# Optimization experiments

Hardware: AMD Instinct MI355X
Metric: run time of the kernel (lower is better)

## Reference

```python
import jax, jax.numpy as jnp
import numpy as np

NUM_EXPERTS = 16
TOP_K = 8
INIT_STD = 0.02

def setup_inputs() -> dict:
    key = jax.random.key(0)
    ks = jax.random.split(key, 5)
    B, S, H, I, E = 2, 2048, 2048, 768, NUM_EXPERTS
    return {
        "hidden_states": jax.random.normal(ks[0], (B, S, H), jnp.float32),
        "w_router": jax.random.normal(ks[1], (H, E), jnp.float32) * INIT_STD,
        "w_gate": jax.random.normal(ks[2], (E, H, I), jnp.float32) * INIT_STD,
        "w_up": jax.random.normal(ks[3], (E, H, I), jnp.float32) * INIT_STD,
        "w_down": jax.random.normal(ks[4], (E, I, H), jnp.float32) * INIT_STD,
    }

def reference(hidden_states, w_router, w_gate, w_up, w_down):
    # Router: logits -> fp32 softmax -> top-k -> renormalize (norm_topk_prob=True)
    router_logits = jnp.einsum("bsh,he->bse", hidden_states, w_router)  # [B,S,E]
    routing_weights = jax.nn.softmax(router_logits.astype(jnp.float32), axis=-1)
    topk_w, topk_idx = jax.lax.top_k(routing_weights, k=TOP_K)  # [B,S,K]
    topk_w = topk_w / topk_w.sum(axis=-1, keepdims=True)
    # Dense per-expert combine weights [B,S,E] (sum over top-k slots matching each expert)
    dense_w = jnp.sum(jax.nn.one_hot(topk_idx, NUM_EXPERTS, dtype=topk_w.dtype) * topk_w[..., None], axis=2)
    dense_w = dense_w.astype(hidden_states.dtype)
    # Every expert runs on all tokens (as in the source loop), vectorized over E
    gate = jax.nn.silu(jnp.einsum("bsh,ehi->besi", hidden_states, w_gate))  # [B,E,S,I]
    up = jnp.einsum("bsh,ehi->besi", hidden_states, w_up)
    expert_out = jnp.einsum("besi,eih->besh", gate * up, w_down)  # [B,E,S,H]
    final = jnp.einsum("bse,besh->bsh", dense_w, expert_out)
    return final, router_logits
```

## Files before the change

kernel.cpp:

```cpp
#include <hip/hip_runtime.h>
#include <hip/hip_bf16.h>


typedef __attribute__((ext_vector_type(8))) short short8;
typedef __attribute__((ext_vector_type(4))) float f32x4;
typedef __attribute__((ext_vector_type(4))) unsigned short us4;

#define NUM_T 4096
#define DH    2048
#define DI    768
#define NE    16
#define DKD   (NE*DI)
#define MAXMT 20
#define HSC_CAP 2560
#define TOK_HALF 2048
#define FINAL_ELEMS ((size_t)NUM_T*DH)


static __device__ __forceinline__ unsigned short f2bf(float f) {
  unsigned int u = __builtin_bit_cast(unsigned int, f);
  u += 0x7fffu + ((u >> 16) & 1u);
  return (unsigned short)(u >> 16);
}

static __device__ __forceinline__ float bf2f(unsigned short b) {
  unsigned int u = ((unsigned int)b) << 16;
  return __builtin_bit_cast(float, u);
}

static __device__ __forceinline__ void gload16(const void* g, void* l) {
  __builtin_amdgcn_global_load_lds(
      (__attribute__((address_space(1))) void*)(g),
      (__attribute__((address_space(3))) void*)(l), 16, 0, 0);
}


__global__ __launch_bounds__(256)
void cvt_hidden_k(const float* __restrict__ in, unsigned short* __restrict__ out) {
  size_t i = (size_t)blockIdx.x * 256 + threadIdx.x;
  const float4* p = (const float4*)in + i * 2;
  float4 a = p[0], b = p[1];
  short8 v;
  v[0] = (short)f2bf(a.x); v[1] = (short)f2bf(a.y);
  v[2] = (short)f2bf(a.z); v[3] = (short)f2bf(a.w);
  v[4] = (short)f2bf(b.x); v[5] = (short)f2bf(b.y);
  v[6] = (short)f2bf(b.z); v[7] = (short)f2bf(b.w);
  *(short8*)(out + i * 8) = v;
}


__global__ __launch_bounds__(256)
void transpose_cvt_k(const float* __restrict__ s0, unsigned short* __restrict__ d0,
                     const float* __restrict__ s1, unsigned short* __restrict__ d1,
                     int C, long inStrideE, long outStrideE, int outLD) {
  __shared__ float tile[128][33];
  const int zz = blockIdx.z, e = zz & 15;
  const float* inE = (zz < 16 ? s0 : s1) + (size_t)e * inStrideE;
  unsigned short* outE = (zz < 16 ? d0 : d1) + (size_t)e * outStrideE;
  const int r0 = blockIdx.x * 128, c0 = blockIdx.y * 32;
  const int tid = threadIdx.x;
  const int lc = tid & 31, rg = tid >> 5;
#pragma unroll
  for (int i = 0; i < 16; i++)
    tile[rg * 16 + i][lc] = inE[(size_t)(r0 + rg * 16 + i) * C + c0 + lc];
  __syncthreads();
  const int u = tid & 31, cg = tid >> 5;
#pragma unroll
  for (int i = 0; i < 4; i++) {
    int c = cg * 4 + i;
    us4 v;
    v[0] = f2bf(tile[u * 4 + 0][c]); v[1] = f2bf(tile[u * 4 + 1][c]);
    v[2] = f2bf(tile[u * 4 + 2][c]); v[3] = f2bf(tile[u * 4 + 3][c]);
    *(us4*)(outE + (size_t)(c0 + c) * outLD + r0 + u * 4) = v;
  }
}


__global__ __launch_bounds__(256)
void router_k(const float* __restrict__ x, const float* __restrict__ wr,
              float* __restrict__ logits_out, unsigned short* __restrict__ dwb,
              unsigned char* __restrict__ slt) {
  int t = blockIdx.x;
  int tid = threadIdx.x, lane = tid & 63, wid = tid >> 6;
  float acc[16];
#pragma unroll
  for (int e = 0; e < 16; e++) acc[e] = 0.f;
  const float* xt = x + (size_t)t * DH;
  for (int i = tid; i < DH; i += 256) {
    float hv = xt[i];
    const float4* w4 = (const float4*)(wr + (size_t)i * 16);
#pragma unroll
    for (int q = 0; q < 4; q++) {
      float4 w = w4[q];
      acc[q * 4 + 0] += hv * w.x; acc[q * 4 + 1] += hv * w.y;
      acc[q * 4 + 2] += hv * w.z; acc[q * 4 + 3] += hv * w.w;
    }
  }
#pragma unroll
  for (int e = 0; e < 16; e++) {
#pragma unroll
    for (int off = 32; off; off >>= 1) acc[e] += __shfl_xor(acc[e], off, 64);
  }
  __shared__ float red[4][16];
  if (lane == 0) {
#pragma unroll
    for (int e = 0; e < 16; e++) red[wid][e] = acc[e];
  }
  __syncthreads();
  if (tid == 0) {
    float lg[16];
#pragma unroll
    for (int e = 0; e < 16; e++) lg[e] = red[0][e] + red[1][e] + red[2][e] + red[3][e];
    float mx = lg[0];
#pragma unroll
    for (int e = 1; e < 16; e++) mx = fmaxf(mx, lg[e]);
    float p[16], s = 0.f;
#pragma unroll
    for (int e = 0; e < 16; e++) { p[e] = __expf(lg[e] - mx); s += p[e]; }
    float inv = 1.f / s;
#pragma unroll
    for (int e = 0; e < 16; e++) p[e] *= inv;
    float tmp[16];
#pragma unroll
    for (int e = 0; e < 16; e++) tmp[e] = p[e];
    int idx[8]; float val[8]; float ts = 0.f;
#pragma unroll
    for (int k = 0; k < 8; k++) {
      int b = 0; float bv = tmp[0];
#pragma unroll
      for (int e = 1; e < 16; e++) { if (tmp[e] > bv) { bv = tmp[e]; b = e; } }
      idx[k] = b; val[k] = bv; tmp[b] = -1.f; ts += bv;
    }
    float dw[16];
    unsigned char sl[16];
#pragma unroll
    for (int e = 0; e < 16; e++) { dw[e] = 0.f; sl[e] = 0xFF; }
    float invt = 1.f / ts;
#pragma unroll
    for (int k = 0; k < 8; k++) { dw[idx[k]] += val[k] * invt; sl[idx[k]] = (unsigned char)k; }
#pragma unroll
    for (int e = 0; e < 16; e++) {
      dwb[(size_t)t * 16 + e] = f2bf(dw[e]);
      slt[(size_t)t * 16 + e] = sl[e];
      logits_out[(size_t)t * 16 + e] = lg[e];
    }
  }
}


__global__ __launch_bounds__(256)
void build_lists_k(const unsigned short* __restrict__ dwb,
                   const unsigned char* __restrict__ slt,
                   unsigned short* __restrict__ lst, int* __restrict__ meta) {
  int e = blockIdx.x;
  int tid = threadIdx.x;
  unsigned short loc[16]; int c = 0;
#pragma unroll
  for (int j = 0; j < 16; j++) {
    int t = tid * 16 + j;
    if (dwb[(size_t)t * 16 + e] != 0) {
      unsigned short s = slt[(size_t)t * 16 + e];
      loc[c++] = (unsigned short)(t | (s << 12));
    }
  }
  __shared__ int sc[256];
  __shared__ int pre[257];
  sc[tid] = c;
  __syncthreads();
  if (tid == 0) {
    int s = 0;
    for (int i = 0; i < 256; i++) { pre[i] = s; s += sc[i]; }
    pre[256] = s;
  }
  __syncthreads();
  unsigned short* L = lst + (size_t)e * NUM_T;
  int base = pre[tid];
  for (int j = 0; j < c; j++) L[base + j] = loc[j];
  int total = pre[256];
  for (int i = total + tid; i < NUM_T; i += 256) L[i] = 0xFFFFu;
  if (tid == 0) { meta[e * 2] = pre[128]; meta[e * 2 + 1] = total; }
}


__global__ __launch_bounds__(256, 3)
void gateup_k(const unsigned short* __restrict__ hbf,
              const unsigned short* __restrict__ wgbt,
              const unsigned short* __restrict__ wubt,
              const unsigned short* __restrict__ dwb,
              const unsigned short* __restrict__ lst,
              unsigned short* __restrict__ hsC) {
  const int bxr = blockIdx.x;
  const int wl  = (bxr & 7) * 480 + (bxr >> 3);
  const int e   = wl / 240;
  const int rem = wl - e * 240;
  const int n0  = (rem / MAXMT) * 64;
  const int m0  = (rem % MAXMT) * 128;

  const unsigned short* L = lst + (size_t)e * NUM_T;
  if (L[m0] & 0x8000) return;

  const int tid = threadIdx.x, lane = tid & 63, wid = tid >> 6;
  const int wm = wid >> 1, wn = wid & 1;
  const int lr = lane & 15, lgp = lane >> 4;

  __shared__ alignas(16) unsigned short As [3 * 128 * 32];
  __shared__ alignas(16) unsigned short Bgs[3 *  64 * 32];
  __shared__ alignas(16) unsigned short Bus[3 *  64 * 32];

  f32x4 zero = {0.f, 0.f, 0.f, 0.f};
  f32x4 accg[4][2], accu[4][2];
#pragma unroll
  for (int m = 0; m < 4; m++)
#pragma unroll
    for (int n = 0; n < 2; n++) { accg[m][n] = zero; accu[m][n] = zero; }

  const unsigned short* wgE = wgbt + (size_t)e * DI * DH;
  const unsigned short* wuE = wubt + (size_t)e * DI * DH;

  const int srow    = lane >> 2;
  const int schunk8 = (((lane & 3) - ((lane >> 3) & 3)) & 3) * 8;

  const int ar0 = m0 + wid * 32 + srow, ar1 = ar0 + 16;
  const unsigned short t0 = L[ar0], t1 = L[ar1];
  const size_t prow0 = (t0 & 0x8000) ? 0 : (size_t)(t0 & 0xFFF);
  const size_t prow1 = (t1 & 0x8000) ? 0 : (size_t)(t1 & 0xFFF);
  const size_t brow = (size_t)(n0 + wid * 16 + srow);

  const int slot8 = (((lane >> 4) + ((lane >> 1) & 3)) & 3) * 8;

  auto stage = [&](int b, int k0) {
    unsigned short* Ab = As  + b * 4096 + wid * 1024;
    unsigned short* Gb = Bgs + b * 2048 + wid * 512;
    unsigned short* Ub = Bus + b * 2048 + wid * 512;
    gload16(hbf + prow0 * DH + k0 + schunk8, Ab);
    gload16(hbf + prow1 * DH + k0 + schunk8, Ab + 512);
    gload16(wgE + brow  * DH + k0 + schunk8, Gb);
    gload16(wuE + brow  * DH + k0 + schunk8, Ub);
  };

  auto compute = [&](int b) {
    const unsigned short* Ab = As  + b * 4096;
    const unsigned short* Gb = Bgs + b * 2048;
    const unsigned short* Ub = Bus + b * 2048;
    short8 a[4], bg[2], bu[2];
#pragma unroll
    for (int m = 0; m < 4; m++)
      a[m] = *(const short8*)(Ab + (wm * 64 + m * 16 + lr) * 32 + slot8);
#pragma unroll
    for (int n = 0; n < 2; n++) {
      bg[n] = *(const short8*)(Gb + (wn * 32 + n * 16 + lr) * 32 + slot8);
      bu[n] = *(const short8*)(Bus + b * 2048 + (wn * 32 + n * 16 + lr) * 32 + slot8);
    }
    (void)Ub;
#pragma unroll
    for (int m = 0; m < 4; m++)
#pragma unroll
      for (int n = 0; n < 2; n++) {
        accg[m][n] = __builtin_amdgcn_mfma_f32_16x16x32_bf16(a[m], bg[n], accg[m][n], 0, 0, 0);
        accu[m][n] = __builtin_amdgcn_mfma_f32_16x16x32_bf16(a[m], bu[n], accu[m][n], 0, 0, 0);
      }
  };

  const int NT = DH / 32;
  stage(0, 0);
  stage(1, 32);
  int bc = 0, bs = 2;
#pragma unroll 1
  for (int i = 0; i < NT - 1; ++i) {
    asm volatile("s_waitcnt vmcnt(4)" ::: "memory");
    __builtin_amdgcn_s_barrier();
    __builtin_amdgcn_sched_barrier(0);
    if (i + 2 < NT) stage(bs, (i + 2) * 32);
    compute(bc);
    bc = (bc == 2) ? 0 : bc + 1;
    bs = (bs == 2) ? 0 : bs + 1;
  }
  asm volatile("s_waitcnt vmcnt(0)" ::: "memory");
  __builtin_amdgcn_s_barrier();
  __builtin_amdgcn_sched_barrier(0);
  compute(bc);

#pragma unroll
  for (int m = 0; m < 4; m++) {
#pragma unroll
    for (int r = 0; r < 4; r++) {
      int mrow = m0 + wm * 64 + m * 16 + 4 * lgp + r;
      unsigned short en = L[mrow];
      if (en & 0x8000) continue;
      int tp = en & 0xFFF;
      float w = bf2f(dwb[(size_t)tp * 16 + e]);
#pragma unroll
      for (int n = 0; n < 2; n++) {
        float g = accg[m][n][r], u = accu[m][n][r];
        float sig = 1.f / (1.f + __expf(-g));
        float val = g * sig * u * w;
        hsC[((size_t)e * HSC_CAP + mrow) * DI + n0 + wn * 32 + n * 16 + lr] = f2bf(val);
      }
    }
  }
}


__global__ __launch_bounds__(256, 3)
void down_half_k(const unsigned short* __restrict__ hsC,
                 const unsigned short* __restrict__ wdbt,
                 const unsigned short* __restrict__ lst,
                 const int* __restrict__ meta,
                 unsigned short* __restrict__ slotbuf, int hf) {
  const int bxr = blockIdx.x;
  const int wl  = (bxr & 7) * 320 + (bxr >> 3);
  const int e   = wl / 160;
  const int rem = wl - e * 160;
  const int n0  = (rem / 10) * 128;
  const int m0  = (rem % 10) * 128;

  const int rs = hf ? meta[e * 2] : 0;
  const int re = hf ? meta[e * 2 + 1] : meta[e * 2];
  const int rcount = re - rs;
  if (m0 >= rcount) return;

  const int tid = threadIdx.x, lane = tid & 63, wid = tid >> 6;
  const int wm = wid >> 1, wn = wid & 1;
  const int lr = lane & 15, lgp = lane >> 4;

  __shared__ alignas(16) unsigned short As[3 * 128 * 32];
  __shared__ alignas(16) unsigned short Bs[3 * 128 * 32];

  f32x4 zero = {0.f, 0.f, 0.f, 0.f};
  f32x4 acc[4][4];
#pragma unroll
  for (int m = 0; m < 4; m++)
#pragma unroll
    for (int n = 0; n < 4; n++) acc[m][n] = zero;

  const int srow    = lane >> 2;
  const int schunk8 = (((lane & 3) - ((lane >> 3) & 3)) & 3) * 8;
  const int sOff0   = wid * 1024;
  const int sOff1   = sOff0 + 512;
  const size_t arow0 = (size_t)(e * HSC_CAP + rs + m0 + wid * 32 + srow);
  const size_t arow1 = arow0 + 16;
  const size_t brow0 = (size_t)(n0 + wid * 32 + srow), brow1 = brow0 + 16;
  const int slot8 = (((lane >> 4) + ((lane >> 1) & 3)) & 3) * 8;

  const unsigned short* wdE = wdbt + (size_t)e * DI;

  auto stage = [&](int b, int k0) {
    unsigned short* Ab = As + b * 4096;
    unsigned short* Bb = Bs + b * 4096;
    gload16(hsC + arow0 * DI + k0 + schunk8, Ab + sOff0);
    gload16(hsC + arow1 * DI + k0 + schunk8, Ab + sOff1);
    gload16(wdE + brow0 * DKD + k0 + schunk8, Bb + sOff0);
    gload16(wdE + brow1 * DKD + k0 + schunk8, Bb + sOff1);
  };

  auto compute = [&](int bsel) {
    const unsigned short* Ab = As + bsel * 4096;
    const unsigned short* Bb = Bs + bsel * 4096;
    short8 a[4], b[4];
#pragma unroll
    for (int m = 0; m < 4; m++)
      a[m] = *(const short8*)(Ab + (size_t)(wm * 64 + m * 16 + lr) * 32 + slot8);
#pragma unroll
    for (int n = 0; n < 4; n++)
      b[n] = *(const short8*)(Bb + (size_t)(wn * 64 + n * 16 + lr) * 32 + slot8);
#pragma unroll
    for (int m = 0; m < 4; m++)
#pragma unroll
      for (int n = 0; n < 4; n++)
        acc[m][n] = __builtin_amdgcn_mfma_f32_16x16x32_bf16(a[m], b[n], acc[m][n], 0, 0, 0);
  };

  const int NT = DI / 32;
  stage(0, 0);
  stage(1, 32);
  int bc = 0, bs = 2;
#pragma unroll 1
  for (int i = 0; i < NT - 1; ++i) {
    asm volatile("s_waitcnt vmcnt(4)" ::: "memory");
    __builtin_amdgcn_s_barrier();
    __builtin_amdgcn_sched_barrier(0);
    if (i + 2 < NT) stage(bs, (i + 2) * 32);
    compute(bc);
    bc = (bc == 2) ? 0 : bc + 1;
    bs = (bs == 2) ? 0 : bs + 1;
  }
  asm volatile("s_waitcnt vmcnt(0)" ::: "memory");
  __builtin_amdgcn_s_barrier();
  __builtin_amdgcn_sched_barrier(0);
  compute(bc);

  const unsigned short* L = lst + (size_t)e * NUM_T;
#pragma unroll
  for (int m = 0; m < 4; m++) {
#pragma unroll
    for (int r = 0; r < 4; r++) {
      int gr = m0 + wm * 64 + m * 16 + 4 * lgp + r;
      if (gr >= rcount) continue;
      unsigned short en = L[rs + gr];
      int t  = en & 0xFFF;
      int s  = (en >> 12) & 7;
      int tl = t - hf * TOK_HALF;
#pragma unroll
      for (int n = 0; n < 4; n++)
        slotbuf[((size_t)s * TOK_HALF + tl) * DH + n0 + wn * 64 + n * 16 + lr] =
            f2bf(acc[m][n][r]);
    }
  }
}


__global__ __launch_bounds__(256)
void reduce_half_k(const unsigned short* __restrict__ slotbuf,
                   float* __restrict__ outp, int hf) {
  size_t i  = (size_t)blockIdx.x * 256 + threadIdx.x;
  size_t tl = i >> 8;
  size_t h0 = (i & 255) * 8;
  float sum[8];
#pragma unroll
  for (int j = 0; j < 8; j++) sum[j] = 0.f;
#pragma unroll
  for (int s = 0; s < 8; s++) {
    short8 v = *(const short8*)(slotbuf + ((size_t)s * TOK_HALF + tl) * DH + h0);
#pragma unroll
    for (int j = 0; j < 8; j++) sum[j] += bf2f((unsigned short)v[j]);
  }
  float* o = outp + ((size_t)(hf * TOK_HALF) + tl) * DH + h0;
  float4 o0 = {sum[0], sum[1], sum[2], sum[3]};
  float4 o1 = {sum[4], sum[5], sum[6], sum[7]};
  *(float4*)o = o0;
  *(float4*)(o + 4) = o1;
}


extern "C" void kernel_launch(void* const* d_in, const int* in_sizes, int n_in,
                              void* d_out, int out_size, void* d_ws, size_t ws_size,
                              hipStream_t stream) {
  const float* x  = (const float*)d_in[0];
  const float* wr = (const float*)d_in[1];
  const float* wg = (const float*)d_in[2];
  const float* wu = (const float*)d_in[3];
  const float* wd = (const float*)d_in[4];

  float* outF = (float*)d_out;
  float* outL = outF + FINAL_ELEMS;

  if (ws_size < 180682880ull) return;
  char* ws = (char*)d_ws;
  unsigned short* hbf   = (unsigned short*)(ws);
  unsigned short* wubt  = (unsigned short*)(ws + 16777216);
  unsigned short* hsC   = (unsigned short*)(ws + 67108864);
  unsigned short* wgbt  = (unsigned short*)(ws + 130023424);
  unsigned short* dwb   = (unsigned short*)(ws + 180355072);
  unsigned short* lst   = (unsigned short*)(ws + 180486144);
  unsigned char*  slt   = (unsigned char*) (ws + 180617216);
  int*            meta  = (int*)           (ws + 180682752);
  unsigned short* sbuf  = (unsigned short*)(ws);
  unsigned short* wdbt  = wgbt;

  cvt_hidden_k<<<4096, 256, 0, stream>>>(x, hbf);
  transpose_cvt_k<<<dim3(16, 24, 32), 256, 0, stream>>>(
      wg, wgbt, wu, wubt, 768, (long)2048 * 768, (long)768 * 2048, 2048);
  router_k<<<4096, 256, 0, stream>>>(x, wr, outL, dwb, slt);
  build_lists_k<<<16, 256, 0, stream>>>(dwb, slt, lst, meta);
  gateup_k<<<3840, 256, 0, stream>>>(hbf, wgbt, wubt, dwb, lst, hsC);
  transpose_cvt_k<<<dim3(6, 64, 16), 256, 0, stream>>>(
      wd, wdbt, wd, wdbt, 2048, (long)768 * 2048, 768L, 12288);
  down_half_k<<<2560, 256, 0, stream>>>(hsC, wdbt, lst, meta, sbuf, 0);
  reduce_half_k<<<2048, 256, 0, stream>>>(sbuf, outF, 0);
  down_half_k<<<2560, 256, 0, stream>>>(hsC, wdbt, lst, meta, sbuf, 1);
  reduce_half_k<<<2048, 256, 0, stream>>>(sbuf, outF, 1);
}
```

Measured before the change: 633.0 us.

## Give each wave private LDS tiles and drop block barriers in expert GEMMs

Both expert GEMM kernels now have each wave load only the A and B rows it consumes into its own LDS region, double-buffered per wave. This removes the per-iteration workgroup s_barrier. The cost is duplicated global loads and twice the loads per wave for the shared operand rows. LDS use grows, so launch bounds drop from 3 to 2 blocks per CU, lowering occupancy.

```diff
diff --git a/kernel.cpp b/kernel.cpp
--- a/kernel.cpp
+++ b/kernel.cpp
@@ -182,7 +182,7 @@
 }
 
 
-__global__ __launch_bounds__(256, 3)
+__global__ __launch_bounds__(256, 2)
 void gateup_k(const unsigned short* __restrict__ hbf,
               const unsigned short* __restrict__ wgbt,
               const unsigned short* __restrict__ wubt,
@@ -203,9 +203,12 @@
   const int wm = wid >> 1, wn = wid & 1;
   const int lr = lane & 15, lgp = lane >> 4;
 
-  __shared__ alignas(16) unsigned short As [3 * 128 * 32];
-  __shared__ alignas(16) unsigned short Bgs[3 *  64 * 32];
-  __shared__ alignas(16) unsigned short Bus[3 *  64 * 32];
+  __shared__ alignas(16) unsigned short As [4 * 2 * 2048];
+  __shared__ alignas(16) unsigned short Bgs[4 * 2 * 1024];
+  __shared__ alignas(16) unsigned short Bus[4 * 2 * 1024];
+  unsigned short* myA = As  + wid * 4096;
+  unsigned short* myG = Bgs + wid * 2048;
+  unsigned short* myU = Bus + wid * 2048;
 
   f32x4 zero = {0.f, 0.f, 0.f, 0.f};
   f32x4 accg[4][2], accu[4][2];
@@ -219,39 +222,49 @@
 
   const int srow    = lane >> 2;
   const int schunk8 = (((lane & 3) - ((lane >> 3) & 3)) & 3) * 8;
-
-  const int ar0 = m0 + wid * 32 + srow, ar1 = ar0 + 16;
-  const unsigned short t0 = L[ar0], t1 = L[ar1];
-  const size_t prow0 = (t0 & 0x8000) ? 0 : (size_t)(t0 & 0xFFF);
-  const size_t prow1 = (t1 & 0x8000) ? 0 : (size_t)(t1 & 0xFFF);
-  const size_t brow = (size_t)(n0 + wid * 16 + srow);
-
-  const int slot8 = (((lane >> 4) + ((lane >> 1) & 3)) & 3) * 8;
-
-  auto stage = [&](int b, int k0) {
-    unsigned short* Ab = As  + b * 4096 + wid * 1024;
-    unsigned short* Gb = Bgs + b * 2048 + wid * 512;
-    unsigned short* Ub = Bus + b * 2048 + wid * 512;
-    gload16(hbf + prow0 * DH + k0 + schunk8, Ab);
-    gload16(hbf + prow1 * DH + k0 + schunk8, Ab + 512);
-    gload16(wgE + brow  * DH + k0 + schunk8, Gb);
-    gload16(wuE + brow  * DH + k0 + schunk8, Ub);
+  const int slot8   = (((lane >> 4) + ((lane >> 1) & 3)) & 3) * 8;
+
+  const unsigned short* gA[4];
+#pragma unroll
+  for (int i = 0; i < 4; i++) {
+    unsigned short en = L[m0 + wm * 64 + i * 16 + srow];
+    gA[i] = hbf + (size_t)((en & 0x8000) ? 0 : (en & 0xFFF)) * DH + schunk8;
+  }
+  const unsigned short* gG[2];
+  const unsigned short* gU[2];
+#pragma unroll
+  for (int i = 0; i < 2; i++) {
+    size_t brow = (size_t)(n0 + wn * 32 + i * 16 + srow);
+    gG[i] = wgE + brow * DH + schunk8;
+    gU[i] = wuE + brow * DH + schunk8;
+  }
+
+  auto stage = [&](int buf, int k0) {
+    unsigned short* Ab = myA + buf * 2048;
+    unsigned short* Gb = myG + buf * 1024;
+    unsigned short* Ub = myU + buf * 1024;
+#pragma unroll
+    for (int i = 0; i < 4; i++) gload16(gA[i] + k0, Ab + i * 512);
+#pragma unroll
+    for (int i = 0; i < 2; i++) {
+      gload16(gG[i] + k0, Gb + i * 512);
+      gload16(gU[i] + k0, Ub + i * 512);
+    }
   };
 
-  auto compute = [&](int b) {
-    const unsigned short* Ab = As  + b * 4096;
-    const unsigned short* Gb = Bgs + b * 2048;
-    const unsigned short* Ub = Bus + b * 2048;
+  auto compute = [&](int buf) {
+    const unsigned short* Ab = myA + buf * 2048;
+    const unsigned short* Gb = myG + buf * 1024;
+    const unsigned short* Ub = myU + buf * 1024;
     short8 a[4], bg[2], bu[2];
 #pragma unroll
     for (int m = 0; m < 4; m++)
-      a[m] = *(const short8*)(Ab + (wm * 64 + m * 16 + lr) * 32 + slot8);
+      a[m] = *(const short8*)(Ab + (m * 16 + lr) * 32 + slot8);
 #pragma unroll
     for (int n = 0; n < 2; n++) {
-      bg[n] = *(const short8*)(Gb + (wn * 32 + n * 16 + lr) * 32 + slot8);
-      bu[n] = *(const short8*)(Bus + b * 2048 + (wn * 32 + n * 16 + lr) * 32 + slot8);
-    }
-    (void)Ub;
+      bg[n] = *(const short8*)(Gb + (n * 16 + lr) * 32 + slot8);
+      bu[n] = *(const short8*)(Ub + (n * 16 + lr) * 32 + slot8);
+    }
 #pragma unroll
     for (int m = 0; m < 4; m++)
 #pragma unroll
@@ -264,21 +277,17 @@
   const int NT = DH / 32;
   stage(0, 0);
   stage(1, 32);
-  int bc = 0, bs = 2;
 #pragma unroll 1
   for (int i = 0; i < NT - 1; ++i) {
-    asm volatile("s_waitcnt vmcnt(4)" ::: "memory");
-    __builtin_amdgcn_s_barrier();
+    asm volatile("s_waitcnt vmcnt(8)" ::: "memory");
     __builtin_amdgcn_sched_barrier(0);
-    if (i + 2 < NT) stage(bs, (i + 2) * 32);
-    compute(bc);
-    bc = (bc == 2) ? 0 : bc + 1;
-    bs = (bs == 2) ? 0 : bs + 1;
+    compute(i & 1);
+    __builtin_amdgcn_sched_barrier(0);
+    if (i + 2 < NT) stage(i & 1, (i + 2) * 32);
   }
   asm volatile("s_waitcnt vmcnt(0)" ::: "memory");
-  __builtin_amdgcn_s_barrier();
   __builtin_amdgcn_sched_barrier(0);
-  compute(bc);
+  compute((NT - 1) & 1);
 
 #pragma unroll
   for (int m = 0; m < 4; m++) {
@@ -301,7 +310,7 @@
 }
 
 
-__global__ __launch_bounds__(256, 3)
+__global__ __launch_bounds__(256, 2)
 void down_half_k(const unsigned short* __restrict__ hsC,
                  const unsigned short* __restrict__ wdbt,
                  const unsigned short* __restrict__ lst,
@@ -323,8 +332,10 @@
   const int wm = wid >> 1, wn = wid & 1;
   const int lr = lane & 15, lgp = lane >> 4;
 
-  __shared__ alignas(16) unsigned short As[3 * 128 * 32];
-  __shared__ alignas(16) unsigned short Bs[3 * 128 * 32];
+  __shared__ alignas(16) unsigned short As[4 * 2 * 2048];
+  __shared__ alignas(16) unsigned short Bs[4 * 2 * 2048];
+  unsigned short* myA = As + wid * 4096;
+  unsigned short* myB = Bs + wid * 4096;
 
   f32x4 zero = {0.f, 0.f, 0.f, 0.f};
   f32x4 acc[4][4];
@@ -335,34 +346,40 @@
 
   const int srow    = lane >> 2;
   const int schunk8 = (((lane & 3) - ((lane >> 3) & 3)) & 3) * 8;
-  const int sOff0   = wid * 1024;
-  const int sOff1   = sOff0 + 512;
-  const size_t arow0 = (size_t)(e * HSC_CAP + rs + m0 + wid * 32 + srow);
-  const size_t arow1 = arow0 + 16;
-  const size_t brow0 = (size_t)(n0 + wid * 32 + srow), brow1 = brow0 + 16;
-  const int slot8 = (((lane >> 4) + ((lane >> 1) & 3)) & 3) * 8;
+  const int slot8   = (((lane >> 4) + ((lane >> 1) & 3)) & 3) * 8;
 
   const unsigned short* wdE = wdbt + (size_t)e * DI;
 
-  auto stage = [&](int b, int k0) {
-    unsigned short* Ab = As + b * 4096;
-    unsigned short* Bb = Bs + b * 4096;
-    gload16(hsC + arow0 * DI + k0 + schunk8, Ab + sOff0);
-    gload16(hsC + arow1 * DI + k0 + schunk8, Ab + sOff1);
-    gload16(wdE + brow0 * DKD + k0 + schunk8, Bb + sOff0);
-    gload16(wdE + brow1 * DKD + k0 + schunk8, Bb + sOff1);
+  const unsigned short* gA[4];
+  const unsigned short* gB[4];
+#pragma unroll
+  for (int i = 0; i < 4; i++) {
+    size_t arow = (size_t)(e * HSC_CAP + rs + m0 + wm * 64 + i * 16 + srow);
+    gA[i] = hsC + arow * DI + schunk8;
+    size_t brow = (size_t)(n0 + wn * 64 + i * 16 + srow);
+    gB[i] = wdE + brow * DKD + schunk8;
+  }
+
+  auto stage = [&](int buf, int k0) {
+    unsigned short* Ab = myA + buf * 2048;
+    unsigned short* Bb = myB + buf * 2048;
+#pragma unroll
+    for (int i = 0; i < 4; i++) {
+      gload16(gA[i] + k0, Ab + i * 512);
+      gload16(gB[i] + k0, Bb + i * 512);
+    }
   };
 
-  auto compute = [&](int bsel) {
-    const unsigned short* Ab = As + bsel * 4096;
-    const unsigned short* Bb = Bs + bsel * 4096;
+  auto compute = [&](int buf) {
+    const unsigned short* Ab = myA + buf * 2048;
+    const unsigned short* Bb = myB + buf * 2048;
     short8 a[4], b[4];
 #pragma unroll
     for (int m = 0; m < 4; m++)
-      a[m] = *(const short8*)(Ab + (size_t)(wm * 64 + m * 16 + lr) * 32 + slot8);
+      a[m] = *(const short8*)(Ab + (m * 16 + lr) * 32 + slot8);
 #pragma unroll
     for (int n = 0; n < 4; n++)
-      b[n] = *(const short8*)(Bb + (size_t)(wn * 64 + n * 16 + lr) * 32 + slot8);
+      b[n] = *(const short8*)(Bb + (n * 16 + lr) * 32 + slot8);
 #pragma unroll
     for (int m = 0; m < 4; m++)
 #pragma unroll
@@ -373,21 +390,17 @@
   const int NT = DI / 32;
   stage(0, 0);
   stage(1, 32);
-  int bc = 0, bs = 2;
 #pragma unroll 1
   for (int i = 0; i < NT - 1; ++i) {
-    asm volatile("s_waitcnt vmcnt(4)" ::: "memory");
-    __builtin_amdgcn_s_barrier();
+    asm volatile("s_waitcnt vmcnt(8)" ::: "memory");
     __builtin_amdgcn_sched_barrier(0);
-    if (i + 2 < NT) stage(bs, (i + 2) * 32);
-    compute(bc);
-    bc = (bc == 2) ? 0 : bc + 1;
-    bs = (bs == 2) ? 0 : bs + 1;
+    compute(i & 1);
+    __builtin_amdgcn_sched_barrier(0);
+    if (i + 2 < NT) stage(i & 1, (i + 2) * 32);
   }
   asm volatile("s_waitcnt vmcnt(0)" ::: "memory");
-  __builtin_amdgcn_s_barrier();
   __builtin_amdgcn_sched_barrier(0);
-  compute(bc);
+  compute((NT - 1) & 1);
 
   const unsigned short* L = lst + (size_t)e * NUM_T;
 #pragma unroll
```

Result: slower. 817.8 us (+29.2%).
